# Performance work log

Measured on AMD Instinct MI355X. Metric: run time of the kernel, lower is better.

## Reference

```python
import jax, jax.numpy as jnp
import numpy as np

EPS = 1e-6

def rmsnorm(x, scale):
    return x * jax.lax.rsqrt(jnp.mean(x * x, axis=-1, keepdims=True) + EPS) * scale

def setup_inputs() -> dict:
    key = jax.random.key(0)
    ks = jax.random.split(key, 8)
    B1, B2 = 16, 64
    D, H, A = 8192, 1024, 2          # deter_size, hidden_size, action_size
    S, C, G = 32, 64, 8              # stoch_size, classes, blocks
    sc = 0.02                        # trunc-normal-ish init scale
    f32 = jnp.float32
    return dict(
        deter=jax.random.normal(ks[0], (B1, B2, D), f32),
        stoch=jax.random.normal(ks[1], (B1, B2, S, C), f32),
        action=jax.random.normal(ks[2], (B1, B2, A), f32),
        W1=(jax.random.normal(ks[3], (H, D), f32) * sc),
        b1=jnp.zeros((H,), f32),
        s1=jnp.ones((H,), f32),
        W2=(jax.random.normal(ks[4], (H, S * C), f32) * sc),
        b2=jnp.zeros((H,), f32),
        s2=jnp.ones((H,), f32),
        W3=(jax.random.normal(ks[5], (H, A), f32) * sc),
        b3=jnp.zeros((H,), f32),
        s3=jnp.ones((H,), f32),
        Wb1=(jax.random.normal(ks[6], (G, (3 * G * H + D) // G, D // G), f32) * sc),
        bb1=jnp.zeros((D,), f32),
        sb1=jnp.ones((D,), f32),
        Wb2=(jax.random.normal(ks[7], (G, D // G, 3 * D // G), f32) * sc),
        bb2=jnp.zeros((3 * D,), f32),
    )

def reference(deter, stoch, action, W1, b1, s1, W2, b2, s2, W3, b3, s3, Wb1, bb1, sb1, Wb2, bb2):
    batch_shape = deter.shape[:-1]
    D = deter.shape[-1]
    d = deter.reshape(-1, D)                       # (B, D)
    B = d.shape[0]
    G = Wb1.shape[0]
    H = W1.shape[0]
    s = stoch.reshape(B, -1)                       # (B, S*C)
    a = action.reshape(B, -1)                      # (B, A)
    a = a / jax.lax.stop_gradient(jnp.maximum(1.0, jnp.abs(a)))
    # three parallel Linear + RMSNorm + SiLU branches
    x1 = jax.nn.silu(rmsnorm(d @ W1.T + b1, s1))
    x2 = jax.nn.silu(rmsnorm(s @ W2.T + b2, s2))
    x3 = jax.nn.silu(rmsnorm(a @ W3.T + b3, s3))
    x = jnp.concatenate([x1, x2, x3], axis=-1)     # (B, 3H)
    x = jnp.broadcast_to(x[:, None, :], (B, G, 3 * H))
    x = jnp.concatenate([x, d.reshape(B, G, D // G)], axis=-1)  # (B, G, 3H + D/G)
    # block-diagonal grouped GEMM + RMSNorm + SiLU (dyn_layers=1)
    h = jnp.einsum('bgi,gio->bgo', x, Wb1).reshape(B, D) + bb1
    h = jax.nn.silu(rmsnorm(h, sb1))
    # final block-diagonal GEMM -> 3*D gate pre-activations
    y = jnp.einsum('bgi,gio->bgo', h.reshape(B, G, D // G), Wb2).reshape(B, 3 * D) + bb2
    r, c, u = jnp.split(y.reshape(B, G, -1), 3, axis=-1)        # each (B, G, D/G)
    reset = jax.nn.sigmoid(r.reshape(B, D))
    cand = jnp.tanh(reset * c.reshape(B, D))
    update = jax.nn.sigmoid(u.reshape(B, D) - 1.0)
    next_deter = update * cand + (1.0 - update) * d
    return next_deter.reshape(*batch_shape, D)
```

## Files before the change

### kernel.cpp

```cpp
#include <hip/hip_runtime.h>
#include <stdint.h>

typedef unsigned short ushort_t;
typedef __attribute__((ext_vector_type(8))) short bf16x8;
typedef __attribute__((ext_vector_type(4))) float f32x4;

#define EPS 1e-6f

__device__ __forceinline__ float b2f(ushort_t u) {
    union { uint32_t i; float f; } v; v.i = ((uint32_t)u) << 16; return v.f;
}
__device__ __forceinline__ ushort_t f2b(float f) {
    union { float f; uint32_t i; } v; v.f = f;
    uint32_t x = v.i;
    uint32_t r = (x + 0x7fffu + ((x >> 16) & 1u)) >> 16;
    return (ushort_t)r;
}

__device__ __forceinline__ void async_copy16(const void* g, void* l) {
    __builtin_amdgcn_global_load_lds(
        (const __attribute__((address_space(1))) uint32_t*)(uintptr_t)g,
        (__attribute__((address_space(3))) uint32_t*)(uintptr_t)l,
        16, 0, 0);
}

__global__ __launch_bounds__(256) void cast_f32_bf16_k(const float* __restrict__ src,
                                                       ushort_t* __restrict__ dst, int n4) {
    int i = blockIdx.x * 256 + threadIdx.x;
    if (i >= n4) return;
    float4 v = ((const float4*)src)[i];
    ushort4 o;
    o.x = f2b(v.x); o.y = f2b(v.y); o.z = f2b(v.z); o.w = f2b(v.w);
    ((ushort4*)dst)[i] = o;
}

__global__ __launch_bounds__(256) void zero_f32_k(float* __restrict__ dst, int n4) {
    int i = blockIdx.x * 256 + threadIdx.x;
    if (i >= n4) return;
    ((float4*)dst)[i] = make_float4(0.f, 0.f, 0.f, 0.f);
}

__global__ __launch_bounds__(256) void transpose_cast_k(const float* __restrict__ src,
                                                        ushort_t* __restrict__ dst,
                                                        int R, int C) {
    __shared__ float tile[32][33];
    int bat = blockIdx.z;
    int c0 = blockIdx.x * 32, r0 = blockIdx.y * 32;
    const float* s = src + (size_t)bat * R * C;
    ushort_t* d = dst + (size_t)bat * R * C;
    int tx = threadIdx.x, ty = threadIdx.y;
    float4 v = *(const float4*)&s[(size_t)(r0 + ty) * C + c0 + tx * 4];
    tile[ty][tx * 4 + 0] = v.x;
    tile[ty][tx * 4 + 1] = v.y;
    tile[ty][tx * 4 + 2] = v.z;
    tile[ty][tx * 4 + 3] = v.w;
    __syncthreads();
    ushort4 o;
    o.x = f2b(tile[tx * 4 + 0][ty]);
    o.y = f2b(tile[tx * 4 + 1][ty]);
    o.z = f2b(tile[tx * 4 + 2][ty]);
    o.w = f2b(tile[tx * 4 + 3][ty]);
    *(ushort4*)&d[(size_t)(c0 + ty) * R + r0 + tx * 4] = o;
}

template <int MODE, bool OUT_BF16, bool ATOMIC>
__global__ __launch_bounds__(256) void gemm_bt_k(
    const ushort_t* __restrict__ Aa, const ushort_t* __restrict__ Ab,
    const ushort_t* __restrict__ Bw,
    float* __restrict__ Cf, ushort_t* __restrict__ Cb,
    int lda, int ldb, int ldc, int Ksl, int k0base) {
    __shared__ __align__(16) ushort_t As[128 * 32];
    __shared__ __align__(16) ushort_t Bs[128 * 32];
    const int tid = threadIdx.x;
    const int bm = blockIdx.x, bn = blockIdx.y, bz = blockIdx.z;
    const int k0 = k0base + bz * Ksl;
    const int m0 = bm * 128, n0 = bn * 128;
    const int lane = tid & 63, w = tid >> 6;
    const int wm = (w & 1) * 64, wn = (w >> 1) * 64;

    f32x4 acc[4][4];
#pragma unroll
    for (int i = 0; i < 4; i++)
#pragma unroll
        for (int j = 0; j < 4; j++) acc[i][j] = (f32x4){0.f, 0.f, 0.f, 0.f};

    const int r0a = tid >> 2;
    const int cslot = tid & 3;
    const int gca = (cslot ^ ((r0a >> 1) & 3)) * 8;
    const int lca = cslot * 8;

    auto a_ptr = [&](int m, int kk) -> const ushort_t* {
        if (MODE == 0) {
            return Aa + (size_t)m * lda + kk;
        } else if (MODE == 1) {
            if (kk < 3072) return Aa + (size_t)m * 3072 + kk;
            int g = n0 >> 10;
            return Ab + (size_t)m * 8192 + g * 1024 + (kk - 3072);
        } else {
            int g = n0 / 3072;
            return Aa + (size_t)m * 8192 + g * 1024 + kk;
        }
    };

    for (int kt = 0; kt < Ksl; kt += 32) {
        const int kk = k0 + kt;
        __syncthreads();
        async_copy16(a_ptr(m0 + r0a, kk + gca), &As[r0a * 32 + lca]);
        async_copy16(a_ptr(m0 + 64 + r0a, kk + gca), &As[(64 + r0a) * 32 + lca]);
        async_copy16(Bw + (size_t)(n0 + r0a) * ldb + kk + gca, &Bs[r0a * 32 + lca]);
        async_copy16(Bw + (size_t)(n0 + 64 + r0a) * ldb + kk + gca, &Bs[(64 + r0a) * 32 + lca]);
        __syncthreads();

        const int qc = lane >> 4;
        bf16x8 af[4], bfr[4];
#pragma unroll
        for (int i = 0; i < 4; i++) {
            int ra = wm + i * 16 + (lane & 15);
            int slot = qc ^ ((ra >> 1) & 3);
            af[i] = *(const bf16x8*)&As[ra * 32 + slot * 8];
        }
#pragma unroll
        for (int j = 0; j < 4; j++) {
            int rb = wn + j * 16 + (lane & 15);
            int slot = qc ^ ((rb >> 1) & 3);
            bfr[j] = *(const bf16x8*)&Bs[rb * 32 + slot * 8];
        }
#pragma unroll
        for (int i = 0; i < 4; i++)
#pragma unroll
            for (int j = 0; j < 4; j++)
                acc[i][j] = __builtin_amdgcn_mfma_f32_16x16x32_bf16(af[i], bfr[j], acc[i][j], 0, 0, 0);
    }

    const int cr = (lane >> 4) * 4, cc = lane & 15;
#pragma unroll
    for (int i = 0; i < 4; i++) {
#pragma unroll
        for (int j = 0; j < 4; j++) {
#pragma unroll
            for (int r = 0; r < 4; r++) {
                int row = m0 + wm + i * 16 + cr + r;
                int col = n0 + wn + j * 16 + cc;
                float v = acc[i][j][r];
                if (ATOMIC) {
                    atomicAdd(&Cf[(size_t)row * ldc + col], v);
                } else if (OUT_BF16) {
                    Cb[(size_t)row * ldc + col] = f2b(v);
                } else {
                    Cf[(size_t)row * ldc + col] = v;
                }
            }
        }
    }
}

__global__ __launch_bounds__(256) void branch3_k(const float* __restrict__ act,
                                                 const float* __restrict__ W3,
                                                 float* __restrict__ xpre) {
    int idx = blockIdx.x * 256 + threadIdx.x;
    int b = idx >> 10, h = idx & 1023;
    float a0 = act[b * 2 + 0], a1 = act[b * 2 + 1];
    a0 = a0 / fmaxf(1.f, fabsf(a0));
    a1 = a1 / fmaxf(1.f, fabsf(a1));
    float v = a0 * W3[h * 2 + 0] + a1 * W3[h * 2 + 1];
    xpre[(size_t)b * 3072 + 2048 + h] = v;
}

__global__ __launch_bounds__(256) void norm_silu_1024_k(
    const float* __restrict__ xpre,
    const float* __restrict__ b1, const float* __restrict__ s1,
    const float* __restrict__ b2, const float* __restrict__ s2,
    const float* __restrict__ b3, const float* __restrict__ s3,
    ushort_t* __restrict__ xbf) {
    int b = blockIdx.x, c = blockIdx.y, tid = threadIdx.x;
    const float* bias = (c == 0) ? b1 : (c == 1) ? b2 : b3;
    const float* scl  = (c == 0) ? s1 : (c == 1) ? s2 : s3;
    const float* src = xpre + (size_t)b * 3072 + c * 1024;
    float4 v = ((const float4*)src)[tid];
    float4 bb = ((const float4*)bias)[tid];
    v.x += bb.x; v.y += bb.y; v.z += bb.z; v.w += bb.w;
    float ss = v.x * v.x + v.y * v.y + v.z * v.z + v.w * v.w;
#pragma unroll
    for (int off = 32; off > 0; off >>= 1) ss += __shfl_down(ss, off, 64);
    __shared__ float wsum[4];
    int lane = tid & 63, wid = tid >> 6;
    if (lane == 0) wsum[wid] = ss;
    __syncthreads();
    float tot = wsum[0] + wsum[1] + wsum[2] + wsum[3];
    float rms = rsqrtf(tot * (1.0f / 1024.0f) + EPS);
    float4 sc = ((const float4*)scl)[tid];
    float o0 = v.x * rms * sc.x; o0 = o0 / (1.f + __expf(-o0));
    float o1 = v.y * rms * sc.y; o1 = o1 / (1.f + __expf(-o1));
    float o2 = v.z * rms * sc.z; o2 = o2 / (1.f + __expf(-o2));
    float o3 = v.w * rms * sc.w; o3 = o3 / (1.f + __expf(-o3));
    ushort4 o; o.x = f2b(o0); o.y = f2b(o1); o.z = f2b(o2); o.w = f2b(o3);
    ((ushort4*)(xbf + (size_t)b * 3072 + c * 1024))[tid] = o;
}

__global__ __launch_bounds__(256) void norm_silu_8192_k(const float* __restrict__ hpre,
                                                        const float* __restrict__ bb1,
                                                        const float* __restrict__ sb1,
                                                        ushort_t* __restrict__ hbf) {
    int b = blockIdx.x, tid = threadIdx.x;
    const float4* src = (const float4*)(hpre + (size_t)b * 8192);
    float4 v[8];
    float ss = 0.f;
#pragma unroll
    for (int k = 0; k < 8; k++) {
        float4 t = src[tid + k * 256];
        float4 bv = ((const float4*)bb1)[tid + k * 256];
        t.x += bv.x; t.y += bv.y; t.z += bv.z; t.w += bv.w;
        v[k] = t;
        ss += t.x * t.x + t.y * t.y + t.z * t.z + t.w * t.w;
    }
#pragma unroll
    for (int off = 32; off > 0; off >>= 1) ss += __shfl_down(ss, off, 64);
    __shared__ float wsum[4];
    int lane = tid & 63, wid = tid >> 6;
    if (lane == 0) wsum[wid] = ss;
    __syncthreads();
    float tot = wsum[0] + wsum[1] + wsum[2] + wsum[3];
    float rms = rsqrtf(tot * (1.0f / 8192.0f) + EPS);
    ushort_t* dst = hbf + (size_t)b * 8192;
#pragma unroll
    for (int k = 0; k < 8; k++) {
        float4 sv = ((const float4*)sb1)[tid + k * 256];
        float o0 = v[k].x * rms * sv.x; o0 = o0 / (1.f + __expf(-o0));
        float o1 = v[k].y * rms * sv.y; o1 = o1 / (1.f + __expf(-o1));
        float o2 = v[k].z * rms * sv.z; o2 = o2 / (1.f + __expf(-o2));
        float o3 = v[k].w * rms * sv.w; o3 = o3 / (1.f + __expf(-o3));
        ushort4 o; o.x = f2b(o0); o.y = f2b(o1); o.z = f2b(o2); o.w = f2b(o3);
        ((ushort4*)dst)[tid + k * 256] = o;
    }
}

__global__ __launch_bounds__(256) void gates_k(const ushort_t* __restrict__ y,
                                               const float* __restrict__ bb2,
                                               const float* __restrict__ deter,
                                               float* __restrict__ out) {
    int idx = blockIdx.x * 256 + threadIdx.x;
    int f = idx * 4;
    int b = f >> 13, d = f & 8191;
    int g = d >> 10, j = d & 1023;
    size_t ybase = (size_t)b * 24576 + g * 3072 + j;
    ushort4 rv = *(const ushort4*)(y + ybase);
    ushort4 cv = *(const ushort4*)(y + ybase + 1024);
    ushort4 uv = *(const ushort4*)(y + ybase + 2048);
    float4 bbr = *(const float4*)(bb2 + g * 3072 + j);
    float4 bbc = *(const float4*)(bb2 + g * 3072 + 1024 + j);
    float4 bbu = *(const float4*)(bb2 + g * 3072 + 2048 + j);
    float4 dv = *(const float4*)(deter + f);
    float rr[4] = {b2f(rv.x) + bbr.x, b2f(rv.y) + bbr.y, b2f(rv.z) + bbr.z, b2f(rv.w) + bbr.w};
    float cc[4] = {b2f(cv.x) + bbc.x, b2f(cv.y) + bbc.y, b2f(cv.z) + bbc.z, b2f(cv.w) + bbc.w};
    float uu[4] = {b2f(uv.x) + bbu.x, b2f(uv.y) + bbu.y, b2f(uv.z) + bbu.z, b2f(uv.w) + bbu.w};
    float dd[4] = {dv.x, dv.y, dv.z, dv.w};
    float oo[4];
#pragma unroll
    for (int t = 0; t < 4; t++) {
        float reset = 1.f / (1.f + __expf(-rr[t]));
        float cand = tanhf(reset * cc[t]);
        float upd = 1.f / (1.f + __expf(-(uu[t] - 1.f)));
        oo[t] = upd * cand + (1.f - upd) * dd[t];
    }
    float4 o; o.x = oo[0]; o.y = oo[1]; o.z = oo[2]; o.w = oo[3];
    *(float4*)(out + f) = o;
}

extern "C" void kernel_launch(void* const* d_in, const int* in_sizes, int n_in,
                              void* d_out, int out_size, void* d_ws, size_t ws_size,
                              hipStream_t stream) {
    const float* deter = (const float*)d_in[0];
    const float* stoch = (const float*)d_in[1];
    const float* action = (const float*)d_in[2];
    const float* W1 = (const float*)d_in[3];
    const float* b1 = (const float*)d_in[4];
    const float* s1 = (const float*)d_in[5];
    const float* W2 = (const float*)d_in[6];
    const float* b2 = (const float*)d_in[7];
    const float* s2 = (const float*)d_in[8];
    const float* W3 = (const float*)d_in[9];
    const float* b3 = (const float*)d_in[10];
    const float* s3 = (const float*)d_in[11];
    const float* Wb1 = (const float*)d_in[12];
    const float* bb1 = (const float*)d_in[13];
    const float* sb1 = (const float*)d_in[14];
    const float* Wb2 = (const float*)d_in[15];
    const float* bb2 = (const float*)d_in[16];
    float* out = (float*)d_out;

    char* ws = (char*)d_ws;
    ushort_t* dbf  = (ushort_t*)(ws + 0);
    ushort_t* sbf  = (ushort_t*)(ws + 16777216);
    ushort_t* W1bf = (ushort_t*)(ws + 20971520);
    ushort_t* W2bf = (ushort_t*)(ws + 37748736);
    ushort_t* Wb1T = (ushort_t*)(ws + 41943040);
    ushort_t* Wb2T = (ushort_t*)(ws + 109051904);
    float*    xpre = (float*)   (ws + 159383552);
    ushort_t* xbf  = (ushort_t*)(ws + 171966464);
    float*    hpre = (float*)   (ws + 178257920);
    ushort_t* hbf  = (ushort_t*)(ws + 211812352);
    ushort_t* ybf  = (ushort_t*)(ws + 228589568);

    cast_f32_bf16_k<<<8192, 256, 0, stream>>>(deter, dbf, 2097152);
    cast_f32_bf16_k<<<2048, 256, 0, stream>>>(stoch, sbf, 524288);
    cast_f32_bf16_k<<<8192, 256, 0, stream>>>(W1, W1bf, 2097152);
    cast_f32_bf16_k<<<2048, 256, 0, stream>>>(W2, W2bf, 524288);
    transpose_cast_k<<<dim3(32, 128, 8), dim3(8, 32), 0, stream>>>(Wb1, Wb1T, 4096, 1024);
    transpose_cast_k<<<dim3(96, 32, 8), dim3(8, 32), 0, stream>>>(Wb2, Wb2T, 1024, 3072);
    zero_f32_k<<<3072, 256, 0, stream>>>(xpre, 786432);

    gemm_bt_k<0, false, true><<<dim3(8, 8, 4), 256, 0, stream>>>(
        dbf, nullptr, W1bf, xpre, nullptr, 8192, 8192, 3072, 2048, 0);
    gemm_bt_k<0, false, true><<<dim3(8, 8, 2), 256, 0, stream>>>(
        sbf, nullptr, W2bf, xpre + 1024, nullptr, 2048, 2048, 3072, 1024, 0);
    branch3_k<<<4096, 256, 0, stream>>>(action, W3, xpre);

    norm_silu_1024_k<<<dim3(1024, 3), 256, 0, stream>>>(xpre, b1, s1, b2, s2, b3, s3, xbf);

    gemm_bt_k<1, false, false><<<dim3(8, 64, 1), 256, 0, stream>>>(
        xbf, dbf, Wb1T, hpre, nullptr, 0, 4096, 8192, 4096, 0);

    norm_silu_8192_k<<<1024, 256, 0, stream>>>(hpre, bb1, sb1, hbf);

    gemm_bt_k<2, true, false><<<dim3(8, 192, 1), 256, 0, stream>>>(
        hbf, nullptr, Wb2T, nullptr, ybf, 0, 1024, 24576, 1024, 0);

    gates_k<<<8192, 256, 0, stream>>>(ybf, bb2, deter, out);
}
```

Measured before the change: 715.7 us.

## Double-buffer GEMM LDS tiles with K=64 and remap block order

Moves the bf16 MFMA GEMM to double-buffered LDS tiles with a K-step of 64 instead of 32. The next tile's async global-to-LDS copy is issued before computing on the current one, so load latency overlaps with MFMA work and there are fewer barriers per K. It also changes the XOR swizzle to 8 slots and remaps block indices so consecutive blocks share B-column tiles for better cache reuse. This doubles LDS use to 64 KB per block, which may lower occupancy. The remap also assumes gridDim.x is 8 and Ksl is a multiple of 64.

```diff
diff --git a/kernel.cpp b/kernel.cpp
--- a/kernel.cpp
+++ b/kernel.cpp
@@ -69,10 +69,16 @@
     const ushort_t* __restrict__ Bw,
     float* __restrict__ Cf, ushort_t* __restrict__ Cb,
     int lda, int ldb, int ldc, int Ksl, int k0base) {
-    __shared__ __align__(16) ushort_t As[128 * 32];
-    __shared__ __align__(16) ushort_t Bs[128 * 32];
+    __shared__ __align__(16) ushort_t As[2][128 * 64];
+    __shared__ __align__(16) ushort_t Bs[2][128 * 64];
     const int tid = threadIdx.x;
-    const int bm = blockIdx.x, bn = blockIdx.y, bz = blockIdx.z;
+
+    const int nxy = gridDim.x * gridDim.y;
+    const int flat = blockIdx.x + (blockIdx.y << 3);
+    const int cpx = nxy >> 3;
+    const int L = (flat & 7) * cpx + (flat >> 3);
+    const int bm = L & 7, bn = L >> 3;
+    const int bz = blockIdx.z;
     const int k0 = k0base + bz * Ksl;
     const int m0 = bm * 128, n0 = bn * 128;
     const int lane = tid & 63, w = tid >> 6;
@@ -83,11 +89,6 @@
     for (int i = 0; i < 4; i++)
 #pragma unroll
         for (int j = 0; j < 4; j++) acc[i][j] = (f32x4){0.f, 0.f, 0.f, 0.f};
-
-    const int r0a = tid >> 2;
-    const int cslot = tid & 3;
-    const int gca = (cslot ^ ((r0a >> 1) & 3)) * 8;
-    const int lca = cslot * 8;
 
     auto a_ptr = [&](int m, int kk) -> const ushort_t* {
         if (MODE == 0) {
@@ -102,34 +103,57 @@
         }
     };
 
-    for (int kt = 0; kt < Ksl; kt += 32) {
-        const int kk = k0 + kt;
-        __syncthreads();
-        async_copy16(a_ptr(m0 + r0a, kk + gca), &As[r0a * 32 + lca]);
-        async_copy16(a_ptr(m0 + 64 + r0a, kk + gca), &As[(64 + r0a) * 32 + lca]);
-        async_copy16(Bw + (size_t)(n0 + r0a) * ldb + kk + gca, &Bs[r0a * 32 + lca]);
-        async_copy16(Bw + (size_t)(n0 + 64 + r0a) * ldb + kk + gca, &Bs[(64 + r0a) * 32 + lca]);
-        __syncthreads();
-
-        const int qc = lane >> 4;
-        bf16x8 af[4], bfr[4];
-#pragma unroll
-        for (int i = 0; i < 4; i++) {
-            int ra = wm + i * 16 + (lane & 15);
-            int slot = qc ^ ((ra >> 1) & 3);
-            af[i] = *(const bf16x8*)&As[ra * 32 + slot * 8];
-        }
-#pragma unroll
-        for (int j = 0; j < 4; j++) {
-            int rb = wn + j * 16 + (lane & 15);
-            int slot = qc ^ ((rb >> 1) & 3);
-            bfr[j] = *(const bf16x8*)&Bs[rb * 32 + slot * 8];
-        }
-#pragma unroll
-        for (int i = 0; i < 4; i++)
-#pragma unroll
-            for (int j = 0; j < 4; j++)
-                acc[i][j] = __builtin_amdgcn_mfma_f32_16x16x32_bf16(af[i], bfr[j], acc[i][j], 0, 0, 0);
+    const int srow = tid >> 3;
+    const int sslot = tid & 7;
+    const int gco = (sslot ^ (srow & 7)) << 3;
+    const int lco = sslot << 3;
+
+    auto stage = [&](int buf, int kk) {
+#pragma unroll
+        for (int p = 0; p < 4; ++p) {
+            int r = (p << 5) + srow;
+            async_copy16(a_ptr(m0 + r, kk + gco), &As[buf][r * 64 + lco]);
+            async_copy16(Bw + (size_t)(n0 + r) * ldb + kk + gco, &Bs[buf][r * 64 + lco]);
+        }
+    };
+
+    const int nt = Ksl >> 6;
+    stage(0, k0);
+    __syncthreads();
+
+    const int qc = lane >> 4;
+    const int rl = lane & 15;
+    int cur = 0;
+
+    for (int t = 0; t < nt; ++t) {
+        if (t + 1 < nt) stage(cur ^ 1, k0 + ((t + 1) << 6));
+
+#pragma unroll
+        for (int h = 0; h < 2; ++h) {
+            bf16x8 af[4], bfr[4];
+#pragma unroll
+            for (int i = 0; i < 4; i++) {
+                int ra = wm + i * 16 + rl;
+                int slot = ((h << 2) + qc) ^ (ra & 7);
+                af[i] = *(const bf16x8*)&As[cur][ra * 64 + (slot << 3)];
+            }
+#pragma unroll
+            for (int j = 0; j < 4; j++) {
+                int rb = wn + j * 16 + rl;
+                int slot = ((h << 2) + qc) ^ (rb & 7);
+                bfr[j] = *(const bf16x8*)&Bs[cur][rb * 64 + (slot << 3)];
+            }
+#pragma unroll
+            for (int i = 0; i < 4; i++)
+#pragma unroll
+                for (int j = 0; j < 4; j++)
+                    acc[i][j] = __builtin_amdgcn_mfma_f32_16x16x32_bf16(af[i], bfr[j], acc[i][j], 0, 0, 0);
+        }
+
+        if (t + 1 < nt) {
+            __syncthreads();
+            cur ^= 1;
+        }
     }
 
     const int cr = (lane >> 4) * 4, cc = lane & 15;
```

Measured after the change: 634.0 us. 11.4% less time.
